# Optimization experiments

Hardware: AMD Instinct MI355X
Metric: run time of the kernel (lower is better)

The kernel has to match this reference:

```python
import jax, jax.numpy as jnp
import numpy as np

N_NODES = 100000
N_EDGES = 3200000
STATE_DIM = 128
HIDDEN = 256
ACTION_DIM = 64
BN_EPS = 1e-5


def setup_inputs() -> dict:
    key = jax.random.key(0)
    ks = jax.random.split(key, 12)
    feat = jax.random.normal(ks[0], (N_NODES, STATE_DIM), dtype=jnp.float32)
    src = jax.random.randint(ks[1], (N_EDGES,), 0, N_NODES, dtype=jnp.int64) if jax.config.jax_enable_x64 else jax.random.randint(ks[1], (N_EDGES,), 0, N_NODES).astype(jnp.int32)
    dst = jax.random.randint(ks[2], (N_EDGES,), 0, N_NODES).astype(src.dtype)
    def glorot(k, shape):
        lim = np.sqrt(6.0 / (shape[0] + shape[1]))
        return jax.random.uniform(k, shape, jnp.float32, -lim, lim)
    W1 = glorot(ks[3], (STATE_DIM, HIDDEN)); b1 = jnp.zeros((HIDDEN,), jnp.float32)
    W2 = glorot(ks[4], (HIDDEN, HIDDEN));   b2 = jnp.zeros((HIDDEN,), jnp.float32)
    g1 = jnp.ones((HIDDEN,), jnp.float32);  be1 = jnp.zeros((HIDDEN,), jnp.float32)
    g2 = jnp.ones((HIDDEN,), jnp.float32);  be2 = jnp.zeros((HIDDEN,), jnp.float32)
    Wa = glorot(ks[5], (HIDDEN, ACTION_DIM)); ba = jnp.zeros((ACTION_DIM,), jnp.float32)
    Wv = glorot(ks[6], (HIDDEN, 1));          bv = jnp.zeros((1,), jnp.float32)
    return {"feat": feat, "src": src, "dst": dst, "W1": W1, "b1": b1, "g1": g1, "be1": be1,
            "W2": W2, "b2": b2, "g2": g2, "be2": be2, "Wa": Wa, "ba": ba, "Wv": Wv, "bv": bv}


def _graph_conv(x, src, dst, dnorm_out, dnorm_in, W, b):
    # DGL GraphConv, norm='both': scale by out-deg^{-1/2} at src, sum-aggregate at dst,
    # scale by in-deg^{-1/2}, then linear.
    m = x * dnorm_out[:, None]                     # [N, F]
    agg = jax.ops.segment_sum(m[src], dst, num_segments=N_NODES)  # SpMM
    h = agg * dnorm_in[:, None]
    return h @ W + b


def _bn_relu(x, gamma, beta):
    mu = x.mean(axis=0)
    var = x.var(axis=0)  # biased, matches torch BN training normalization
    return jax.nn.relu((x - mu) * jax.lax.rsqrt(var + BN_EPS) * gamma + beta)


def reference(feat, src, dst, W1, b1, g1, be1, W2, b2, g2, be2, Wa, ba, Wv, bv):
    ones = jnp.ones((src.shape[0],), feat.dtype)
    deg_out = jax.ops.segment_sum(ones, src, num_segments=N_NODES)
    deg_in = jax.ops.segment_sum(ones, dst, num_segments=N_NODES)
    dnorm_out = jax.lax.rsqrt(jnp.clip(deg_out, 1.0))
    dnorm_in = jax.lax.rsqrt(jnp.clip(deg_in, 1.0))
    h = _bn_relu(_graph_conv(feat, src, dst, dnorm_out, dnorm_in, W1, b1), g1, be1)
    h = _bn_relu(_graph_conv(h, src, dst, dnorm_out, dnorm_in, W2, b2), g2, be2)
    adv = h @ Wa + ba                              # [N, A]
    val = h @ Wv + bv                              # [N, 1]
    Q = val + (adv - adv.mean(axis=1, keepdims=True))
    return Q
```

## Files before the change

### kernel.cpp

```cpp
#include <hip/hip_runtime.h>
#include <hip/hip_bf16.h>

#define NN 100000
#define NE 3200000
#define HID 256
#define SDIM 128
#define ADIM 64
#define BN_EPS 1e-5f

#define BSH 9
#define NB 196
#define EPB 16384
#define NAB 196
#define CAP 24576

typedef __attribute__((ext_vector_type(8))) short short8;
typedef __attribute__((ext_vector_type(4))) float f32x4;

__device__ __forceinline__ void atomAdd(float* p, float v) { unsafeAtomicAdd(p, v); }
__device__ __forceinline__ float bf2f(ushort u) {
    union { unsigned i; float f; } c; c.i = ((unsigned)u) << 16; return c.f;
}
__device__ __forceinline__ ushort f2bf(float x) {
    __hip_bfloat16 h = __float2bfloat16(x);
    return *reinterpret_cast<ushort*>(&h);
}

__global__ __launch_bounds__(1024)
void k_hist(const int* __restrict__ src, const int* __restrict__ dst,
            unsigned* __restrict__ gh_d, unsigned* __restrict__ gh_s, int E) {
    __shared__ unsigned hd[NB], hs[NB];
    int tid = threadIdx.x;
    if (tid < NB) { hd[tid] = 0; hs[tid] = 0; }
    __syncthreads();
    int base = blockIdx.x * EPB;
    int cnt = min(EPB, E - base);
    for (int i = tid; i < cnt; i += 1024) {
        atomicAdd(&hd[dst[base + i] >> BSH], 1u);
        atomicAdd(&hs[src[base + i] >> BSH], 1u);
    }
    __syncthreads();
    if (tid < NB) {
        if (hd[tid]) atomicAdd(&gh_d[tid * 16], hd[tid]);
        if (hs[tid]) atomicAdd(&gh_s[tid * 16], hs[tid]);
    }
}

__global__ __launch_bounds__(256)
void k_scan_b(const unsigned* __restrict__ gh_d, const unsigned* __restrict__ gh_s,
              unsigned* __restrict__ gcur_d, unsigned* __restrict__ gcur_s,
              unsigned* __restrict__ bbase_d, unsigned* __restrict__ bbase_s,
              int* __restrict__ row_ptr) {
    __shared__ unsigned v[256];
    int t = threadIdx.x;
    unsigned x = (t < NB) ? gh_d[t * 16] : 0;
    v[t] = x; __syncthreads();
    for (int off = 1; off < 256; off <<= 1) {
        unsigned a = (t >= off) ? v[t - off] : 0;
        __syncthreads(); v[t] += a; __syncthreads();
    }
    if (t < NB) { bbase_d[t] = v[t] - x; gcur_d[t * 16] = v[t] - x; }
    if (t == 255) { bbase_d[NB] = v[255]; row_ptr[NN] = (int)v[255]; }
    __syncthreads();
    unsigned y = (t < NB) ? gh_s[t * 16] : 0;
    v[t] = y; __syncthreads();
    for (int off = 1; off < 256; off <<= 1) {
        unsigned a = (t >= off) ? v[t - off] : 0;
        __syncthreads(); v[t] += a; __syncthreads();
    }
    if (t < NB) { bbase_s[t] = v[t] - y; gcur_s[t * 16] = v[t] - y; }
    if (t == 255) bbase_s[NB] = v[255];
}

__global__ __launch_bounds__(1024)
void k_part(const int* __restrict__ src, const int* __restrict__ dst,
            unsigned* __restrict__ gcur_d, unsigned* __restrict__ gcur_s,
            unsigned* __restrict__ outd, ushort* __restrict__ outs, int E) {
    __shared__ unsigned hd[NB], hs[NB], ld_[NB], ls_[NB], cd[NB], cs[NB], bd[NB], bs[NB];
    __shared__ unsigned sv[256];
    __shared__ unsigned stage_d[EPB];
    __shared__ ushort stage_s[EPB];
    __shared__ unsigned char sbd[EPB], sbs[EPB];
    const int tid = threadIdx.x;
    const int base = blockIdx.x * EPB;
    const int cnt = min(EPB, E - base);
    if (tid < NB) { hd[tid] = 0; hs[tid] = 0; }
    __syncthreads();

    int es[16], ed[16];
    #pragma unroll
    for (int i = 0; i < 16; ++i) {
        int g = tid + i * 1024;
        if (g < cnt) { es[i] = src[base + g]; ed[i] = dst[base + g]; }
        else { es[i] = -1; ed[i] = -1; }
    }
    #pragma unroll
    for (int i = 0; i < 16; ++i)
        if (ed[i] >= 0) {
            atomicAdd(&hd[ed[i] >> BSH], 1u);
            atomicAdd(&hs[es[i] >> BSH], 1u);
        }
    __syncthreads();

    {
        unsigned x = (tid < NB) ? hd[tid] : 0;
        if (tid < 256) sv[tid] = x;
        __syncthreads();
        for (int off = 1; off < 256; off <<= 1) {
            unsigned a = 0;
            if (tid < 256 && tid >= off) a = sv[tid - off];
            __syncthreads();
            if (tid < 256) sv[tid] += a;
            __syncthreads();
        }
        if (tid < NB) {
            ld_[tid] = sv[tid] - x; cd[tid] = sv[tid] - x;
            bd[tid] = atomicAdd(&gcur_d[tid * 16], hd[tid]);
        }
        __syncthreads();
        unsigned y = (tid < NB) ? hs[tid] : 0;
        if (tid < 256) sv[tid] = y;
        __syncthreads();
        for (int off = 1; off < 256; off <<= 1) {
            unsigned a = 0;
            if (tid < 256 && tid >= off) a = sv[tid - off];
            __syncthreads();
            if (tid < 256) sv[tid] += a;
            __syncthreads();
        }
        if (tid < NB) {
            ls_[tid] = sv[tid] - y; cs[tid] = sv[tid] - y;
            bs[tid] = atomicAdd(&gcur_s[tid * 16], hs[tid]);
        }
        __syncthreads();
    }

    #pragma unroll
    for (int i = 0; i < 16; ++i)
        if (ed[i] >= 0) {
            int b = ed[i] >> BSH;
            unsigned p = atomicAdd(&cd[b], 1u);
            stage_d[p] = ((unsigned)(ed[i] & ((1 << BSH) - 1)) << 17) | (unsigned)es[i];
            sbd[p] = (unsigned char)b;
            int b2 = es[i] >> BSH;
            unsigned p2 = atomicAdd(&cs[b2], 1u);
            stage_s[p2] = (ushort)(es[i] & ((1 << BSH) - 1));
            sbs[p2] = (unsigned char)b2;
        }
    __syncthreads();

    for (int i = tid; i < cnt; i += 1024) {
        unsigned b = sbd[i];
        outd[bd[b] + (unsigned)i - ld_[b]] = stage_d[i];
        unsigned b2 = sbs[i];
        outs[bs[b2] + (unsigned)i - ls_[b2]] = stage_s[i];
    }
}

__global__ __launch_bounds__(1024)
void k_csr(const unsigned* __restrict__ outd, const unsigned* __restrict__ bbase_d,
           int* __restrict__ row_ptr, int* __restrict__ csr_src, float* __restrict__ dni) {
    __shared__ unsigned h[512], sc[512];
    __shared__ int sorted[CAP];
    const int tid = threadIdx.x, b = blockIdx.x;
    const unsigned beg = bbase_d[b], end = bbase_d[b + 1];
    const int cnt = (int)(end - beg);
    if (tid < 512) h[tid] = 0;
    __syncthreads();
    for (int i = tid; i < cnt; i += 1024) atomicAdd(&h[outd[beg + i] >> 17], 1u);
    __syncthreads();
    unsigned my = 0;
    if (tid < 512) { my = h[tid]; sc[tid] = my; }
    __syncthreads();
    for (int off = 1; off < 512; off <<= 1) {
        unsigned a = 0;
        if (tid < 512 && tid >= off) a = sc[tid - off];
        __syncthreads();
        if (tid < 512) sc[tid] += a;
        __syncthreads();
    }
    const int n0 = b << BSH;
    const int nb = min(512, NN - n0);
    unsigned excl = 0;
    if (tid < 512) excl = sc[tid] - my;
    __syncthreads();
    if (tid < 512) h[tid] = excl;
    if (tid < nb) {
        row_ptr[n0 + tid] = (int)(beg + excl);
        dni[n0 + tid] = rsqrtf(fmaxf((float)my, 1.0f));
    }
    __syncthreads();
    for (int i = tid; i < cnt; i += 1024) {
        unsigned p = outd[beg + i];
        unsigned pos = atomicAdd(&h[p >> 17], 1u);
        sorted[pos] = (int)(p & 0x1FFFFu);
    }
    __syncthreads();
    for (int i = tid; i < cnt; i += 1024) csr_src[beg + i] = sorted[i];
}

__global__ __launch_bounds__(1024)
void k_degout(const ushort* __restrict__ outs, const unsigned* __restrict__ bbase_s,
              float* __restrict__ dno) {
    __shared__ unsigned h[512];
    const int tid = threadIdx.x, b = blockIdx.x;
    const unsigned beg = bbase_s[b], end = bbase_s[b + 1];
    const int cnt = (int)(end - beg);
    if (tid < 512) h[tid] = 0;
    __syncthreads();
    for (int i = tid; i < cnt; i += 1024) atomicAdd(&h[outs[beg + i]], 1u);
    __syncthreads();
    const int n0 = b << BSH;
    const int nb = min(512, NN - n0);
    if (tid < nb) dno[n0 + tid] = rsqrtf(fmaxf((float)h[tid], 1.0f));
}

__global__ __launch_bounds__(256)
void k_wt(const float* __restrict__ W, ushort* __restrict__ Wt, int K, int N) {
    int idx = blockIdx.x * 256 + threadIdx.x;
    if (idx >= K * N) return;
    int n = idx / K, k = idx - n * K;
    Wt[idx] = f2bf(W[(size_t)k * N + n]);
}

__global__ __launch_bounds__(256)
void k_prescale_cvt(const float* __restrict__ X, const float* __restrict__ dno,
                    ushort* __restrict__ Y, int total4) {
    int idx = blockIdx.x * 256 + threadIdx.x;
    if (idx >= total4) return;
    int row = idx >> 5;
    float s = dno[row];
    float4 v = reinterpret_cast<const float4*>(X)[idx];
    ushort4 o;
    o.x = f2bf(v.x * s); o.y = f2bf(v.y * s);
    o.z = f2bf(v.z * s); o.w = f2bf(v.w * s);
    reinterpret_cast<ushort4*>(Y)[idx] = o;
}

template <int F>
__global__ __launch_bounds__(256)
void k_spmm_bf16(const int* __restrict__ row_ptr, const int* __restrict__ csr_src,
                 const ushort* __restrict__ X, const float* __restrict__ dni,
                 ushort* __restrict__ Y, int N) {
    const int node = blockIdx.x * 4 + (threadIdx.x >> 6);
    if (node >= N) return;
    const int lane = threadIdx.x & 63;
    const int beg = row_ptr[node];
    const int end = row_ptr[node + 1];
    float acc[4] = {0.f, 0.f, 0.f, 0.f};

    if (F == 256) {
        const ushort* Xl = X + lane * 4;
        int e = beg;
        for (; e + 1 < end; e += 2) {
            int s0 = csr_src[e];
            int s1 = csr_src[e + 1];
            ushort4 v0 = *reinterpret_cast<const ushort4*>(Xl + (size_t)s0 * 256);
            ushort4 v1 = *reinterpret_cast<const ushort4*>(Xl + (size_t)s1 * 256);
            acc[0] += bf2f(v0.x) + bf2f(v1.x);
            acc[1] += bf2f(v0.y) + bf2f(v1.y);
            acc[2] += bf2f(v0.z) + bf2f(v1.z);
            acc[3] += bf2f(v0.w) + bf2f(v1.w);
        }
        if (e < end) {
            int s0 = csr_src[e];
            ushort4 v0 = *reinterpret_cast<const ushort4*>(Xl + (size_t)s0 * 256);
            acc[0] += bf2f(v0.x); acc[1] += bf2f(v0.y);
            acc[2] += bf2f(v0.z); acc[3] += bf2f(v0.w);
        }
        float wi = dni[node];
        ushort4 o;
        o.x = f2bf(acc[0] * wi); o.y = f2bf(acc[1] * wi);
        o.z = f2bf(acc[2] * wi); o.w = f2bf(acc[3] * wi);
        *reinterpret_cast<ushort4*>(Y + (size_t)node * 256 + lane * 4) = o;
    } else {
        const int half = lane >> 5;
        const int l = lane & 31;
        const ushort* Xl = X + l * 4;
        for (int e = beg + half; e < end; e += 2) {
            int s = csr_src[e];
            ushort4 v = *reinterpret_cast<const ushort4*>(Xl + (size_t)s * 128);
            acc[0] += bf2f(v.x); acc[1] += bf2f(v.y);
            acc[2] += bf2f(v.z); acc[3] += bf2f(v.w);
        }
        acc[0] += __shfl_xor(acc[0], 32);
        acc[1] += __shfl_xor(acc[1], 32);
        acc[2] += __shfl_xor(acc[2], 32);
        acc[3] += __shfl_xor(acc[3], 32);
        if (half == 0) {
            float wi = dni[node];
            ushort4 o;
            o.x = f2bf(acc[0] * wi); o.y = f2bf(acc[1] * wi);
            o.z = f2bf(acc[2] * wi); o.w = f2bf(acc[3] * wi);
            *reinterpret_cast<ushort4*>(Y + (size_t)node * 128 + l * 4) = o;
        }
    }
}

template <int K>
__global__ __launch_bounds__(256)
void k_gemm_mfma(const ushort* __restrict__ A, const ushort* __restrict__ Wt,
                 const float* __restrict__ bias, ushort* __restrict__ outb,
                 float* __restrict__ stats, int M) {
    __shared__ ushort As[128][40];
    __shared__ ushort Bs[64][40];
    __shared__ float sred[4][2][64];
    const int tid = threadIdx.x;
    const int w = tid >> 6;
    const int lane = tid & 63;
    const int row0 = blockIdx.x * 128;
    const int col0 = blockIdx.y * 64;
    f32x4 acc[2][4] = {};

    const int arow = lane & 15;
    const int ak = (lane >> 4) * 8;

    for (int k0 = 0; k0 < K; k0 += 32) {
        #pragma unroll
        for (int h = 0; h < 2; ++h) {
            int r = (tid >> 2) + 64 * h;
            int kk = (tid & 3) * 8;
            int row = row0 + r;
            int4 v = make_int4(0, 0, 0, 0);
            if (row < M) v = *reinterpret_cast<const int4*>(A + (size_t)row * K + k0 + kk);
            *reinterpret_cast<int4*>(&As[r][kk]) = v;
        }
        {
            int n = tid >> 2;
            int kk = (tid & 3) * 8;
            int4 v = *reinterpret_cast<const int4*>(Wt + (size_t)(col0 + n) * K + k0 + kk);
            *reinterpret_cast<int4*>(&Bs[n][kk]) = v;
        }
        __syncthreads();

        short8 afr[2], bfr[4];
        #pragma unroll
        for (int mi = 0; mi < 2; ++mi)
            afr[mi] = *reinterpret_cast<const short8*>(&As[w * 32 + mi * 16 + arow][ak]);
        #pragma unroll
        for (int ni = 0; ni < 4; ++ni)
            bfr[ni] = *reinterpret_cast<const short8*>(&Bs[ni * 16 + arow][ak]);
        #pragma unroll
        for (int mi = 0; mi < 2; ++mi)
            #pragma unroll
            for (int ni = 0; ni < 4; ++ni)
                acc[mi][ni] = __builtin_amdgcn_mfma_f32_16x16x32_bf16(afr[mi], bfr[ni], acc[mi][ni], 0, 0, 0);
        __syncthreads();
    }

    const int ncol = lane & 15;
    const int rbase = (lane >> 4) * 4;
    float s1l[4], s2l[4];
    #pragma unroll
    for (int ni = 0; ni < 4; ++ni) { s1l[ni] = 0.f; s2l[ni] = 0.f; }
    #pragma unroll
    for (int ni = 0; ni < 4; ++ni) {
        int col = col0 + ni * 16 + ncol;
        float b = bias[col];
        #pragma unroll
        for (int mi = 0; mi < 2; ++mi) {
            #pragma unroll
            for (int q = 0; q < 4; ++q) {
                int row = row0 + w * 32 + mi * 16 + rbase + q;
                if (row < M) {
                    float val = acc[mi][ni][q] + b;
                    outb[(size_t)row * HID + col] = f2bf(val);
                    s1l[ni] += val;
                    s2l[ni] += val * val;
                }
            }
        }
    }
    #pragma unroll
    for (int ni = 0; ni < 4; ++ni) {
        s1l[ni] += __shfl_xor(s1l[ni], 16);
        s1l[ni] += __shfl_xor(s1l[ni], 32);
        s2l[ni] += __shfl_xor(s2l[ni], 16);
        s2l[ni] += __shfl_xor(s2l[ni], 32);
        if ((lane >> 4) == 0) {
            sred[w][0][ni * 16 + ncol] = s1l[ni];
            sred[w][1][ni * 16 + ncol] = s2l[ni];
        }
    }
    __syncthreads();
    if (tid < 128) {
        int c = tid & 63, st = tid >> 6;
        float v = sred[0][st][c] + sred[1][st][c] + sred[2][st][c] + sred[3][st][c];
        atomAdd(&stats[st * HID + col0 + c], v);
    }
}

__global__ __launch_bounds__(256)
void k_bn_relu_ps(const ushort* __restrict__ Gb, const float* __restrict__ stats,
                  const float* __restrict__ gamma, const float* __restrict__ beta,
                  const float* __restrict__ dno, ushort* __restrict__ Y, int total8) {
    int idx = blockIdx.x * 256 + threadIdx.x;
    if (idx >= total8) return;
    int row = idx >> 5;
    int c0 = (idx & 31) * 8;
    short8 v = *reinterpret_cast<const short8*>(Gb + (size_t)idx * 8);
    float s = dno[row];
    float inv_n = 1.0f / (float)NN;
    short8 o;
    #pragma unroll
    for (int j = 0; j < 8; ++j) {
        int c = c0 + j;
        float mean = stats[c] * inv_n;
        float var = stats[HID + c] * inv_n - mean * mean;
        float sc = gamma[c] * rsqrtf(var + BN_EPS);
        float sh = beta[c] - mean * sc;
        float x = bf2f((ushort)v[j]);
        float y = fmaf(x, sc, sh);
        y = y > 0.f ? y : 0.f;
        o[j] = (short)f2bf(y * s);
    }
    *reinterpret_cast<short8*>(Y + (size_t)idx * 8) = o;
}

__global__ __launch_bounds__(256)
void k_bn_qhead(const ushort* __restrict__ Gb, const float* __restrict__ stats,
                const float* __restrict__ gamma, const float* __restrict__ beta,
                const float* __restrict__ Wa, const float* __restrict__ ba,
                const float* __restrict__ Wv, const float* __restrict__ bv,
                float* __restrict__ out, int M) {
    __shared__ float sc_s[HID], sh_s[HID];
    __shared__ float hs[16][HID];
    __shared__ float advs[16][64];
    __shared__ float vparts[16][16];
    __shared__ float means[16], vals[16];
    int tid = threadIdx.x;
    int base = blockIdx.x * 16;
    {
        float inv_n = 1.0f / (float)NN;
        float mean = stats[tid] * inv_n;
        float var = stats[HID + tid] * inv_n - mean * mean;
        float sc = gamma[tid] * rsqrtf(var + BN_EPS);
        sc_s[tid] = sc;
        sh_s[tid] = beta[tid] - mean * sc;
    }
    __syncthreads();
    #pragma unroll
    for (int it = 0; it < 2; ++it) {
        int slot = tid + it * 256;
        int r = slot >> 5, c8 = slot & 31;
        int row = base + r;
        short8 v = {};
        if (row < M) v = *reinterpret_cast<const short8*>(Gb + (size_t)row * HID + c8 * 8);
        #pragma unroll
        for (int j = 0; j < 8; ++j) {
            int c = c8 * 8 + j;
            float x = (row < M) ? bf2f((ushort)v[j]) : 0.f;
            float y = fmaf(x, sc_s[c], sh_s[c]);
            hs[r][c] = y > 0.f ? y : 0.f;
        }
    }
    __syncthreads();
    int col = tid & 63, rg = tid >> 6;
    float b = ba[col];
    float acc[4] = {b, b, b, b};
    for (int k = 0; k < HID; ++k) {
        float w = Wa[k * ADIM + col];
        #pragma unroll
        for (int i = 0; i < 4; ++i) acc[i] = fmaf(hs[rg * 4 + i][k], w, acc[i]);
    }
    #pragma unroll
    for (int i = 0; i < 4; ++i) advs[rg * 4 + i][col] = acc[i];
    int r = tid >> 4, p = tid & 15;
    float vp = 0.f;
    #pragma unroll
    for (int k = 0; k < 16; ++k) vp += hs[r][p * 16 + k] * Wv[p * 16 + k];
    vparts[r][p] = vp;
    __syncthreads();
    if (tid < 16) {
        float s = 0.f;
        #pragma unroll
        for (int c = 0; c < ADIM; ++c) s += advs[tid][c];
        means[tid] = s * (1.0f / ADIM);
        float v = bv[0];
        #pragma unroll
        for (int q = 0; q < 16; ++q) v += vparts[tid][q];
        vals[tid] = v;
    }
    __syncthreads();
    #pragma unroll
    for (int i = 0; i < 4; ++i) {
        int rr = rg * 4 + i;
        int row = base + rr;
        if (row < M) out[(size_t)row * ADIM + col] = vals[rr] + advs[rr][col] - means[rr];
    }
}

extern "C" void kernel_launch(void* const* d_in, const int* in_sizes, int n_in,
                              void* d_out, int out_size, void* d_ws, size_t ws_size,
                              hipStream_t stream) {
    const float* feat = (const float*)d_in[0];
    const int* src = (const int*)d_in[1];
    const int* dst = (const int*)d_in[2];
    const float* W1 = (const float*)d_in[3];
    const float* b1 = (const float*)d_in[4];
    const float* g1 = (const float*)d_in[5];
    const float* be1 = (const float*)d_in[6];
    const float* W2 = (const float*)d_in[7];
    const float* b2 = (const float*)d_in[8];
    const float* g2 = (const float*)d_in[9];
    const float* be2 = (const float*)d_in[10];
    const float* Wa = (const float*)d_in[11];
    const float* ba = (const float*)d_in[12];
    const float* Wv = (const float*)d_in[13];
    const float* bv = (const float*)d_in[14];
    float* out = (float*)d_out;

    char* w = (char*)d_ws;
    unsigned* gh_d   = (unsigned*)w;  w += (size_t)NB * 16 * 4;
    unsigned* gh_s   = (unsigned*)w;  w += (size_t)NB * 16 * 4;
    float* stats     = (float*)w;     w += 1024 * 4;
    unsigned* gcur_d = (unsigned*)w;  w += (size_t)NB * 16 * 4;
    unsigned* gcur_s = (unsigned*)w;  w += (size_t)NB * 16 * 4;
    unsigned* bbase_d= (unsigned*)w;  w += (NB + 4) * 4;
    unsigned* bbase_s= (unsigned*)w;  w += (NB + 4) * 4;
    float* dn_out    = (float*)w;     w += (size_t)NN * 4;
    float* dn_in     = (float*)w;     w += (size_t)NN * 4;
    int* row_ptr     = (int*)w;       w += (size_t)(NN + 4) * 4;
    unsigned* outd   = (unsigned*)w;  w += (size_t)NE * 4;
    ushort* outs     = (ushort*)w;    w += (size_t)NE * 2;
    int* csr_src     = (int*)w;       w += (size_t)NE * 4;
    ushort* Wt1      = (ushort*)w;    w += (size_t)HID * SDIM * 2;
    ushort* Wt2      = (ushort*)w;    w += (size_t)HID * HID * 2;
    ushort* Xb       = (ushort*)w;    w += (size_t)NN * HID * 2;
    ushort* Ab       = (ushort*)w;    w += (size_t)NN * HID * 2;
    ushort* Gb       = (ushort*)w;    w += (size_t)NN * HID * 2;

    hipMemsetAsync(gh_d, 0, (size_t)2 * NB * 16 * 4 + 1024 * 4, stream);

    k_hist<<<NAB, 1024, 0, stream>>>(src, dst, gh_d, gh_s, NE);
    k_scan_b<<<1, 256, 0, stream>>>(gh_d, gh_s, gcur_d, gcur_s, bbase_d, bbase_s, row_ptr);
    k_part<<<NAB, 1024, 0, stream>>>(src, dst, gcur_d, gcur_s, outd, outs, NE);
    k_csr<<<NB, 1024, 0, stream>>>(outd, bbase_d, row_ptr, csr_src, dn_in);
    k_degout<<<NB, 1024, 0, stream>>>(outs, bbase_s, dn_out);

    k_wt<<<(SDIM * HID + 255) / 256, 256, 0, stream>>>(W1, Wt1, SDIM, HID);
    k_wt<<<(HID * HID + 255) / 256, 256, 0, stream>>>(W2, Wt2, HID, HID);

    {
        int t4 = NN * (SDIM / 4);
        k_prescale_cvt<<<(t4 + 255) / 256, 256, 0, stream>>>(feat, dn_out, Xb, t4);
        k_spmm_bf16<SDIM><<<(NN + 3) / 4, 256, 0, stream>>>(row_ptr, csr_src, Xb, dn_in, Ab, NN);
        dim3 grid((NN + 127) / 128, HID / 64);
        k_gemm_mfma<SDIM><<<grid, 256, 0, stream>>>(Ab, Wt1, b1, Gb, stats, NN);
        int t8 = NN * (HID / 8);
        k_bn_relu_ps<<<(t8 + 255) / 256, 256, 0, stream>>>(Gb, stats, g1, be1, dn_out, Xb, t8);
    }

    {
        k_spmm_bf16<HID><<<(NN + 3) / 4, 256, 0, stream>>>(row_ptr, csr_src, Xb, dn_in, Ab, NN);
        dim3 grid((NN + 127) / 128, HID / 64);
        k_gemm_mfma<HID><<<grid, 256, 0, stream>>>(Ab, Wt2, b2, Gb, stats + 512, NN);
        k_bn_qhead<<<(NN + 15) / 16, 256, 0, stream>>>(Gb, stats + 512, g2, be2, Wa, ba, Wv, bv, out, NN);
    }
}
```

Measured before the change: 831.0 us.

## Use MFMA for Q-head and widen GEMM tiles to full hidden width

The Q-head kernel now packs Wa and Wv into one bf16 transposed matrix of 80 columns. It computes advantages and value with MFMA over 128-row tiles, fusing BN+ReLU into the A-tile load and doing the row mean with lane shuffles. This replaces the scalar FMA loop over 16-row blocks. The hidden-layer GEMM now computes all 256 output columns per block instead of 64, so each A tile is loaded from global memory once rather than four times. The cost is a larger accumulator footprint per thread, which may raise register pressure and lower occupancy.

```diff
diff --git a/kernel.cpp b/kernel.cpp
--- a/kernel.cpp
+++ b/kernel.cpp
@@ -221,6 +221,18 @@
     if (idx >= K * N) return;
     int n = idx / K, k = idx - n * K;
     Wt[idx] = f2bf(W[(size_t)k * N + n]);
+}
+
+__global__ __launch_bounds__(256)
+void k_wth(const float* __restrict__ Wa, const float* __restrict__ Wv,
+           ushort* __restrict__ Wh) {
+    int idx = blockIdx.x * 256 + threadIdx.x;
+    if (idx >= 80 * HID) return;
+    int n = idx / HID, k = idx - n * HID;
+    float v = 0.f;
+    if (n < ADIM) v = Wa[(size_t)k * ADIM + n];
+    else if (n == ADIM) v = Wv[k];
+    Wh[idx] = f2bf(v);
 }
 
 __global__ __launch_bounds__(256)
@@ -298,95 +310,95 @@
 }
 
 template <int K>
-__global__ __launch_bounds__(256)
+__global__ __launch_bounds__(256, 2)
 void k_gemm_mfma(const ushort* __restrict__ A, const ushort* __restrict__ Wt,
                  const float* __restrict__ bias, ushort* __restrict__ outb,
                  float* __restrict__ stats, int M) {
     __shared__ ushort As[128][40];
-    __shared__ ushort Bs[64][40];
-    __shared__ float sred[4][2][64];
+    __shared__ ushort Bs[256][40];
+    __shared__ float sred[4][2][128];
     const int tid = threadIdx.x;
     const int w = tid >> 6;
     const int lane = tid & 63;
+    const int wr = (w >> 1) * 64;
+    const int wc = (w & 1) * 128;
     const int row0 = blockIdx.x * 128;
-    const int col0 = blockIdx.y * 64;
-    f32x4 acc[2][4] = {};
-
-    const int arow = lane & 15;
-    const int ak = (lane >> 4) * 8;
+    f32x4 acc[4][8] = {};
+
+    const int frow = lane & 15;
+    const int fk = (lane >> 4) * 8;
 
     for (int k0 = 0; k0 < K; k0 += 32) {
         #pragma unroll
         for (int h = 0; h < 2; ++h) {
-            int r = (tid >> 2) + 64 * h;
-            int kk = (tid & 3) * 8;
+            int slot = tid + 256 * h;
+            int r = slot >> 2;
+            int c = (slot & 3) * 8;
             int row = row0 + r;
             int4 v = make_int4(0, 0, 0, 0);
-            if (row < M) v = *reinterpret_cast<const int4*>(A + (size_t)row * K + k0 + kk);
-            *reinterpret_cast<int4*>(&As[r][kk]) = v;
-        }
-        {
-            int n = tid >> 2;
-            int kk = (tid & 3) * 8;
-            int4 v = *reinterpret_cast<const int4*>(Wt + (size_t)(col0 + n) * K + k0 + kk);
-            *reinterpret_cast<int4*>(&Bs[n][kk]) = v;
-        }
-        __syncthreads();
-
-        short8 afr[2], bfr[4];
-        #pragma unroll
-        for (int mi = 0; mi < 2; ++mi)
-            afr[mi] = *reinterpret_cast<const short8*>(&As[w * 32 + mi * 16 + arow][ak]);
-        #pragma unroll
-        for (int ni = 0; ni < 4; ++ni)
-            bfr[ni] = *reinterpret_cast<const short8*>(&Bs[ni * 16 + arow][ak]);
-        #pragma unroll
-        for (int mi = 0; mi < 2; ++mi)
+            if (row < M) v = *reinterpret_cast<const int4*>(A + (size_t)row * K + k0 + c);
+            *reinterpret_cast<int4*>(&As[r][c]) = v;
+        }
+        #pragma unroll
+        for (int h = 0; h < 4; ++h) {
+            int slot = tid + 256 * h;
+            int n = slot >> 2;
+            int c = (slot & 3) * 8;
+            int4 v = *reinterpret_cast<const int4*>(Wt + (size_t)n * K + k0 + c);
+            *reinterpret_cast<int4*>(&Bs[n][c]) = v;
+        }
+        __syncthreads();
+
+        short8 afr[4], bfr[8];
+        #pragma unroll
+        for (int mi = 0; mi < 4; ++mi)
+            afr[mi] = *reinterpret_cast<const short8*>(&As[wr + mi * 16 + frow][fk]);
+        #pragma unroll
+        for (int ni = 0; ni < 8; ++ni)
+            bfr[ni] = *reinterpret_cast<const short8*>(&Bs[wc + ni * 16 + frow][fk]);
+        #pragma unroll
+        for (int mi = 0; mi < 4; ++mi)
             #pragma unroll
-            for (int ni = 0; ni < 4; ++ni)
+            for (int ni = 0; ni < 8; ++ni)
                 acc[mi][ni] = __builtin_amdgcn_mfma_f32_16x16x32_bf16(afr[mi], bfr[ni], acc[mi][ni], 0, 0, 0);
         __syncthreads();
     }
 
     const int ncol = lane & 15;
     const int rbase = (lane >> 4) * 4;
-    float s1l[4], s2l[4];
-    #pragma unroll
-    for (int ni = 0; ni < 4; ++ni) { s1l[ni] = 0.f; s2l[ni] = 0.f; }
-    #pragma unroll
-    for (int ni = 0; ni < 4; ++ni) {
-        int col = col0 + ni * 16 + ncol;
+    #pragma unroll
+    for (int ni = 0; ni < 8; ++ni) {
+        int col = wc + ni * 16 + ncol;
         float b = bias[col];
-        #pragma unroll
-        for (int mi = 0; mi < 2; ++mi) {
+        float s1 = 0.f, s2 = 0.f;
+        #pragma unroll
+        for (int mi = 0; mi < 4; ++mi) {
             #pragma unroll
             for (int q = 0; q < 4; ++q) {
-                int row = row0 + w * 32 + mi * 16 + rbase + q;
+                int row = row0 + wr + mi * 16 + rbase + q;
                 if (row < M) {
                     float val = acc[mi][ni][q] + b;
                     outb[(size_t)row * HID + col] = f2bf(val);
-                    s1l[ni] += val;
-                    s2l[ni] += val * val;
+                    s1 += val;
+                    s2 += val * val;
                 }
             }
         }
-    }
-    #pragma unroll
-    for (int ni = 0; ni < 4; ++ni) {
-        s1l[ni] += __shfl_xor(s1l[ni], 16);
-        s1l[ni] += __shfl_xor(s1l[ni], 32);
-        s2l[ni] += __shfl_xor(s2l[ni], 16);
-        s2l[ni] += __shfl_xor(s2l[ni], 32);
+        s1 += __shfl_xor(s1, 16); s1 += __shfl_xor(s1, 32);
+        s2 += __shfl_xor(s2, 16); s2 += __shfl_xor(s2, 32);
         if ((lane >> 4) == 0) {
-            sred[w][0][ni * 16 + ncol] = s1l[ni];
-            sred[w][1][ni * 16 + ncol] = s2l[ni];
-        }
-    }
-    __syncthreads();
-    if (tid < 128) {
-        int c = tid & 63, st = tid >> 6;
-        float v = sred[0][st][c] + sred[1][st][c] + sred[2][st][c] + sred[3][st][c];
-        atomAdd(&stats[st * HID + col0 + c], v);
+            sred[w][0][ni * 16 + ncol] = s1;
+            sred[w][1][ni * 16 + ncol] = s2;
+        }
+    }
+    __syncthreads();
+    {
+        int c = tid;
+        int half = c >> 7, cl = c & 127;
+        float v0 = sred[half][0][cl] + sred[half + 2][0][cl];
+        float v1 = sred[half][1][cl] + sred[half + 2][1][cl];
+        atomAdd(&stats[c], v0);
+        atomAdd(&stats[HID + c], v1);
     }
 }
 
@@ -420,16 +432,18 @@
 __global__ __launch_bounds__(256)
 void k_bn_qhead(const ushort* __restrict__ Gb, const float* __restrict__ stats,
                 const float* __restrict__ gamma, const float* __restrict__ beta,
-                const float* __restrict__ Wa, const float* __restrict__ ba,
-                const float* __restrict__ Wv, const float* __restrict__ bv,
-                float* __restrict__ out, int M) {
+                const ushort* __restrict__ Wh, const float* __restrict__ ba,
+                const float* __restrict__ bv, float* __restrict__ out, int M) {
+    __shared__ ushort As[128][40];
+    __shared__ ushort Bs[80][264];
     __shared__ float sc_s[HID], sh_s[HID];
-    __shared__ float hs[16][HID];
-    __shared__ float advs[16][64];
-    __shared__ float vparts[16][16];
-    __shared__ float means[16], vals[16];
-    int tid = threadIdx.x;
-    int base = blockIdx.x * 16;
+    const int tid = threadIdx.x;
+    const int w = tid >> 6;
+    const int lane = tid & 63;
+    const int row0 = blockIdx.x * 128;
+    const int frow = lane & 15;
+    const int fk8 = (lane >> 4) * 8;
+
     {
         float inv_n = 1.0f / (float)NN;
         float mean = stats[tid] * inv_n;
@@ -438,55 +452,81 @@
         sc_s[tid] = sc;
         sh_s[tid] = beta[tid] - mean * sc;
     }
-    __syncthreads();
-    #pragma unroll
-    for (int it = 0; it < 2; ++it) {
-        int slot = tid + it * 256;
-        int r = slot >> 5, c8 = slot & 31;
-        int row = base + r;
-        short8 v = {};
-        if (row < M) v = *reinterpret_cast<const short8*>(Gb + (size_t)row * HID + c8 * 8);
-        #pragma unroll
-        for (int j = 0; j < 8; ++j) {
-            int c = c8 * 8 + j;
-            float x = (row < M) ? bf2f((ushort)v[j]) : 0.f;
-            float y = fmaf(x, sc_s[c], sh_s[c]);
-            hs[r][c] = y > 0.f ? y : 0.f;
-        }
-    }
-    __syncthreads();
-    int col = tid & 63, rg = tid >> 6;
-    float b = ba[col];
-    float acc[4] = {b, b, b, b};
-    for (int k = 0; k < HID; ++k) {
-        float w = Wa[k * ADIM + col];
-        #pragma unroll
-        for (int i = 0; i < 4; ++i) acc[i] = fmaf(hs[rg * 4 + i][k], w, acc[i]);
-    }
-    #pragma unroll
-    for (int i = 0; i < 4; ++i) advs[rg * 4 + i][col] = acc[i];
-    int r = tid >> 4, p = tid & 15;
-    float vp = 0.f;
-    #pragma unroll
-    for (int k = 0; k < 16; ++k) vp += hs[r][p * 16 + k] * Wv[p * 16 + k];
-    vparts[r][p] = vp;
-    __syncthreads();
-    if (tid < 16) {
-        float s = 0.f;
-        #pragma unroll
-        for (int c = 0; c < ADIM; ++c) s += advs[tid][c];
-        means[tid] = s * (1.0f / ADIM);
-        float v = bv[0];
-        #pragma unroll
-        for (int q = 0; q < 16; ++q) v += vparts[tid][q];
-        vals[tid] = v;
-    }
-    __syncthreads();
-    #pragma unroll
-    for (int i = 0; i < 4; ++i) {
-        int rr = rg * 4 + i;
-        int row = base + rr;
-        if (row < M) out[(size_t)row * ADIM + col] = vals[rr] + advs[rr][col] - means[rr];
+    #pragma unroll
+    for (int h = 0; h < 10; ++h) {
+        int slot = tid + 256 * h;
+        int n = slot >> 5;
+        int c = (slot & 31) * 8;
+        int4 v = *reinterpret_cast<const int4*>(Wh + (size_t)n * HID + c);
+        *reinterpret_cast<int4*>(&Bs[n][c]) = v;
+    }
+    __syncthreads();
+
+    f32x4 acc[2][5] = {};
+    for (int k0 = 0; k0 < HID; k0 += 32) {
+        #pragma unroll
+        for (int h = 0; h < 2; ++h) {
+            int slot = tid + 256 * h;
+            int r = slot >> 2;
+            int c = (slot & 3) * 8;
+            int row = row0 + r;
+            short8 o = {};
+            if (row < M) {
+                short8 v = *reinterpret_cast<const short8*>(Gb + (size_t)row * HID + k0 + c);
+                #pragma unroll
+                for (int j = 0; j < 8; ++j) {
+                    int k = k0 + c + j;
+                    float y = fmaf(bf2f((ushort)v[j]), sc_s[k], sh_s[k]);
+                    o[j] = (short)f2bf(y > 0.f ? y : 0.f);
+                }
+            }
+            *reinterpret_cast<short8*>(&As[r][c]) = o;
+        }
+        __syncthreads();
+        short8 afr[2], bfr[5];
+        #pragma unroll
+        for (int mi = 0; mi < 2; ++mi)
+            afr[mi] = *reinterpret_cast<const short8*>(&As[w * 32 + mi * 16 + frow][fk8]);
+        #pragma unroll
+        for (int ni = 0; ni < 5; ++ni)
+            bfr[ni] = *reinterpret_cast<const short8*>(&Bs[ni * 16 + frow][k0 + fk8]);
+        #pragma unroll
+        for (int mi = 0; mi < 2; ++mi)
+            #pragma unroll
+            for (int ni = 0; ni < 5; ++ni)
+                acc[mi][ni] = __builtin_amdgcn_mfma_f32_16x16x32_bf16(afr[mi], bfr[ni], acc[mi][ni], 0, 0, 0);
+        __syncthreads();
+    }
+
+    const int ncol = lane & 15;
+    const int gb = lane & 48;
+    const float bv0 = bv[0];
+    float ba_l[4];
+    #pragma unroll
+    for (int ni = 0; ni < 4; ++ni) ba_l[ni] = ba[ni * 16 + ncol];
+    #pragma unroll
+    for (int mi = 0; mi < 2; ++mi) {
+        #pragma unroll
+        for (int q = 0; q < 4; ++q) {
+            int row = row0 + w * 32 + mi * 16 + (lane >> 4) * 4 + q;
+            float adv[4];
+            float s = 0.f;
+            #pragma unroll
+            for (int ni = 0; ni < 4; ++ni) {
+                adv[ni] = acc[mi][ni][q] + ba_l[ni];
+                s += adv[ni];
+            }
+            s += __shfl_xor(s, 1); s += __shfl_xor(s, 2);
+            s += __shfl_xor(s, 4); s += __shfl_xor(s, 8);
+            float mean = s * (1.0f / ADIM);
+            float val = acc[mi][4][q] + bv0;
+            val = __shfl(val, gb);
+            if (row < M) {
+                #pragma unroll
+                for (int ni = 0; ni < 4; ++ni)
+                    out[(size_t)row * ADIM + ni * 16 + ncol] = val + adv[ni] - mean;
+            }
+        }
     }
 }
 
@@ -526,6 +566,7 @@
     int* csr_src     = (int*)w;       w += (size_t)NE * 4;
     ushort* Wt1      = (ushort*)w;    w += (size_t)HID * SDIM * 2;
     ushort* Wt2      = (ushort*)w;    w += (size_t)HID * HID * 2;
+    ushort* Whb      = (ushort*)w;    w += (size_t)80 * HID * 2;
     ushort* Xb       = (ushort*)w;    w += (size_t)NN * HID * 2;
     ushort* Ab       = (ushort*)w;    w += (size_t)NN * HID * 2;
     ushort* Gb       = (ushort*)w;    w += (size_t)NN * HID * 2;
@@ -540,21 +581,22 @@
 
     k_wt<<<(SDIM * HID + 255) / 256, 256, 0, stream>>>(W1, Wt1, SDIM, HID);
     k_wt<<<(HID * HID + 255) / 256, 256, 0, stream>>>(W2, Wt2, HID, HID);
+    k_wth<<<(80 * HID + 255) / 256, 256, 0, stream>>>(Wa, Wv, Whb);
+
+    const int gblocks = (NN + 127) / 128;
 
     {
         int t4 = NN * (SDIM / 4);
         k_prescale_cvt<<<(t4 + 255) / 256, 256, 0, stream>>>(feat, dn_out, Xb, t4);
         k_spmm_bf16<SDIM><<<(NN + 3) / 4, 256, 0, stream>>>(row_ptr, csr_src, Xb, dn_in, Ab, NN);
-        dim3 grid((NN + 127) / 128, HID / 64);
-        k_gemm_mfma<SDIM><<<grid, 256, 0, stream>>>(Ab, Wt1, b1, Gb, stats, NN);
+        k_gemm_mfma<SDIM><<<gblocks, 256, 0, stream>>>(Ab, Wt1, b1, Gb, stats, NN);
         int t8 = NN * (HID / 8);
         k_bn_relu_ps<<<(t8 + 255) / 256, 256, 0, stream>>>(Gb, stats, g1, be1, dn_out, Xb, t8);
     }
 
     {
         k_spmm_bf16<HID><<<(NN + 3) / 4, 256, 0, stream>>>(row_ptr, csr_src, Xb, dn_in, Ab, NN);
-        dim3 grid((NN + 127) / 128, HID / 64);
-        k_gemm_mfma<HID><<<grid, 256, 0, stream>>>(Ab, Wt2, b2, Gb, stats + 512, NN);
-        k_bn_qhead<<<(NN + 15) / 16, 256, 0, stream>>>(Gb, stats + 512, g2, be2, Wa, ba, Wv, bv, out, NN);
-    }
-}
+        k_gemm_mfma<HID><<<gblocks, 256, 0, stream>>>(Ab, Wt2, b2, Gb, stats + 512, NN);
+        k_bn_qhead<<<gblocks, 256, 0, stream>>>(Gb, stats + 512, g2, be2, Whb, ba, bv, out, NN);
+    }
+}
```

Measured after the change: 740.2 us. -10.9%, faster.
